# Optimization experiments

Measured on AMD Instinct MI355X. Metric: run time of the kernel, lower is better.

Reference implementation:

```python
import jax, jax.numpy as jnp
import numpy as np

B = 65536          # batch
H_DIM, W_DIM = 8, 8  # feather_size tuple
N = H_DIM * W_DIM    # 64 flat features
INNER = (N + 1) ** 2 # 4225 = outer-product size after prepending ones column
EPS = 1e-6


def setup_inputs() -> dict:
    key = jax.random.key(0)
    k1, k2 = jax.random.split(key, 2)
    x = jax.random.normal(k1, (B, N), jnp.float32)
    # nn.Linear(INNER, N): weight [out, in] = [N, INNER]
    W = jax.random.normal(k2, (N, INNER), jnp.float32) / np.sqrt(INNER)
    b = jnp.zeros((N,), jnp.float32)
    gamma = jnp.ones((N,), jnp.float32)   # LayerNorm scale
    beta = jnp.zeros((N,), jnp.float32)   # LayerNorm shift
    return {"x": x, "W": W, "b": b, "gamma": gamma, "beta": beta}


def reference(x, W, b, gamma, beta):
    Bsz = x.shape[0]
    # prepend ones column: [B, N+1]
    ones = jnp.ones((Bsz, 1), x.dtype)
    x1 = jnp.concatenate([ones, x], axis=-1)
    # bmm outer product x1 @ x1^T per row -> [B, N+1, N+1], flatten to [B, INNER]
    outer = (x1[:, :, None] * x1[:, None, :]).reshape(Bsz, INNER)
    # Linear(INNER -> N)
    y = outer @ W.T + b  # [B, N]
    # UER-py LayerNorm: gamma*(y-u)/sqrt(var+eps)+beta over last dim
    u = jnp.mean(y, axis=-1, keepdims=True)
    s = jnp.mean((y - u) ** 2, axis=-1, keepdims=True)
    y = gamma * (y - u) / jnp.sqrt(s + EPS) + beta
    # final view back to the (out) feather matrix shape
    return y.reshape(Bsz, H_DIM, W_DIM)
```

## Files before the change

### kernel.cpp

```cpp
#include <hip/hip_runtime.h>
#include <stdint.h>
#include <stddef.h>

typedef _Float16 f16;
typedef _Float16 f16x2 __attribute__((ext_vector_type(2)));
typedef _Float16 f16x4 __attribute__((ext_vector_type(4)));
typedef _Float16 f16x8 __attribute__((ext_vector_type(8)));
typedef float f32x16 __attribute__((ext_vector_type(16)));

#define INNER_SZ 4225
#define NQ 164
#define XSTR 72

__global__ __launch_bounds__(256) void cm_prep(const float* __restrict__ W,
                                               const float* __restrict__ bias,
                                               f16* __restrict__ Wf2,
                                               float* __restrict__ cvec) {
  int idx = blockIdx.x * 256 + threadIdx.x;
  if (idx < NQ * 1024) {
    int q   = idx >> 10;
    int r10 = idx & 1023;
    int ngh = r10 >> 9;
    int rr  = r10 & 511;
    int G   = rr >> 3;
    int e   = rr & 7;
    int c = G >> 1, hh = G & 1;
    int o = ngh * 32 + c;
    int kl = hh * 8 + e;
    float v = 0.f;
    if (q < 160) {
      int b, start;
      if (q < 16)      { b = 0; start = 0;  }
      else if (q < 48) { b = 1; start = 16; }
      else if (q < 96) { b = 2; start = 48; }
      else             { b = 3; start = 96; }
      int rel = q - start;
      int i = 16 * b + rel / (b + 1);
      int s = rel % (b + 1);
      int j = s * 16 + kl;
      if (j < i)
        v = W[o * INNER_SZ + (i + 1) * 65 + (j + 1)] +
            W[o * INNER_SZ + (j + 1) * 65 + (i + 1)];
      else if (j == i)
        v = W[o * INNER_SZ + (i + 1) * 65 + (i + 1)];
    } else {
      int j = (q - 160) * 16 + kl;
      v = W[o * INNER_SZ + (j + 1)] + W[o * INNER_SZ + (j + 1) * 65];
    }
    Wf2[idx] = (f16)v;
  }
  if (idx < 64) cvec[idx] = W[idx * INNER_SZ] + bias[idx];
}

__device__ __forceinline__ f16x8 mulsp(f16x2 sp, f16x8 wv) {
  f16x8 r;
#pragma unroll
  for (int e = 0; e < 4; ++e)
    ((f16x2*)&r)[e] = sp * ((const f16x2*)&wv)[e];
  return r;
}

template <int QLO>
__device__ __forceinline__ void kbody(f16x8 (&wr)[10], const char* bsrc,
                                      const f16* xs, int r0, int r1,
                                      const f16x8 (&xw0)[4], const f16x8 (&xw1)[4],
                                      f32x16& acc0, f32x16& acc1) {
  f16x2 sp0 = {}, sp1 = {};
#pragma unroll
  for (int qi = 0; qi < 82; ++qi) {
    const int q = QLO + qi;
    int i, s, lin;
    if (q >= 160) { i = 0; s = q - 160; lin = 1; }
    else {
      int b = (q < 16) ? 0 : (q < 48) ? 1 : (q < 96) ? 2 : 3;
      int st = (b == 0) ? 0 : (b == 1) ? 16 : (b == 2) ? 48 : 96;
      int rel = q - st;
      i = 16 * b + rel / (b + 1);
      s = rel % (b + 1);
      lin = 0;
    }
    bool newi = (qi == 0);
    if (qi > 0 && !lin) {
      int qp = q - 1;
      int bp = (qp < 16) ? 0 : (qp < 48) ? 1 : (qp < 96) ? 2 : 3;
      int stp = (bp == 0) ? 0 : (bp == 1) ? 16 : (bp == 2) ? 48 : 96;
      int ip = 16 * bp + (qp - stp) / (bp + 1);
      newi = (ip != i);
    }
    if (!lin && newi) {
      uint32_t u0 = *(const uint16_t*)(xs + r0 * XSTR + i);
      uint32_t u1 = *(const uint16_t*)(xs + r1 * XSTR + i);
      sp0 = __builtin_bit_cast(f16x2, u0 | (u0 << 16));
      sp1 = __builtin_bit_cast(f16x2, u1 | (u1 << 16));
    }
    f16x8 b_ = wr[qi % 10];
    if (qi + 10 < 82)
      wr[qi % 10] = *(const f16x8*)(bsrc + (size_t)(QLO + qi + 10) * 2048);
    f16x8 a0, a1;
    if (lin) { a0 = xw0[s]; a1 = xw1[s]; }
    else     { a0 = mulsp(sp0, xw0[s]); a1 = mulsp(sp1, xw1[s]); }
    acc0 = __builtin_amdgcn_mfma_f32_32x32x16_f16(a0, b_, acc0, 0, 0, 0);
    acc1 = __builtin_amdgcn_mfma_f32_32x32x16_f16(a1, b_, acc1, 0, 0, 0);
  }
}

__global__ __launch_bounds__(512, 4) void cm_main(
    const float* __restrict__ x, const f16* __restrict__ Wf2,
    const float* __restrict__ cvec, const float* __restrict__ gamma,
    const float* __restrict__ beta, float* __restrict__ out) {
  __shared__ __align__(16) union SM {
    f16 xs[128 * XSTR];
    struct { float red[128][64]; float yt[64 * 128]; } e;
  } sm;

  const int tid = threadIdx.x;
  const int lane = tid & 63;
  const int w = tid >> 6;
  const int rowg = w & 1;
  const int ch = (w >> 1) & 1;
  const int seg = w >> 2;
  const int c31 = lane & 31;
  const int h = lane >> 5;
  const long mbase = (long)blockIdx.x * 128;

  const char* bsrc = (const char*)Wf2 + ch * 1024 + (2 * c31 + h) * 16;
  f16x8 wr[10];
  if (seg == 0) {
#pragma unroll
    for (int p = 0; p < 10; ++p)
      wr[p] = *(const f16x8*)(bsrc + (size_t)p * 2048);
  } else {
#pragma unroll
    for (int p = 0; p < 10; ++p)
      wr[p] = *(const f16x8*)(bsrc + (size_t)(82 + p) * 2048);
  }

#pragma unroll
  for (int it = 0; it < 4; ++it) {
    int idx = it * 2048 + tid * 4;
    int row = idx >> 6, col = idx & 63;
    const float4 v = *(const float4*)(x + (size_t)(mbase + row) * 64 + col);
    f16x4 hv = {(f16)v.x, (f16)v.y, (f16)v.z, (f16)v.w};
    *(f16x4*)(sm.xs + row * XSTR + col) = hv;
  }
  __syncthreads();

  const int r0 = rowg * 64 + c31, r1 = rowg * 64 + 32 + c31;
  f16x8 xw0[4], xw1[4];
#pragma unroll
  for (int s = 0; s < 4; ++s) {
    xw0[s] = *(const f16x8*)(sm.xs + r0 * XSTR + s * 16 + h * 8);
    xw1[s] = *(const f16x8*)(sm.xs + r1 * XSTR + s * 16 + h * 8);
  }

  f32x16 acc0 = (f32x16)(0.0f);
  f32x16 acc1 = (f32x16)(0.0f);
  if (seg == 0) kbody<0>(wr, bsrc, sm.xs, r0, r1, xw0, xw1, acc0, acc1);
  else          kbody<82>(wr, bsrc, sm.xs, r0, r1, xw0, xw1, acc0, acc1);

  __syncthreads();
  if (seg == 1) {
#pragma unroll
    for (int r = 0; r < 16; ++r) {
      int rl = (r & 3) + 8 * (r >> 2) + 4 * h;
      sm.e.red[rowg * 64 + rl][ch * 32 + c31] = acc0[r];
      sm.e.red[rowg * 64 + 32 + rl][ch * 32 + c31] = acc1[r];
    }
  }
  __syncthreads();
  if (seg == 0) {
#pragma unroll
    for (int r = 0; r < 16; ++r) {
      int rl = (r & 3) + 8 * (r >> 2) + 4 * h;
      acc0[r] += sm.e.red[rowg * 64 + rl][ch * 32 + c31];
      acc1[r] += sm.e.red[rowg * 64 + 32 + rl][ch * 32 + c31];
    }
    const int cg = ch * 32 + c31;
    const int swz = (c31 & 7) << 4;
#pragma unroll
    for (int rq = 0; rq < 4; ++rq) {
      int b0 = cg * 512 + rowg * 256 + 0 * 128 + rq * 32 + h * 16;
      int b1 = cg * 512 + rowg * 256 + 1 * 128 + rq * 32 + h * 16;
      *(float4*)((char*)sm.e.yt + (b0 ^ swz)) =
          make_float4(acc0[rq * 4 + 0], acc0[rq * 4 + 1], acc0[rq * 4 + 2], acc0[rq * 4 + 3]);
      *(float4*)((char*)sm.e.yt + (b1 ^ swz)) =
          make_float4(acc1[rq * 4 + 0], acc1[rq * 4 + 1], acc1[rq * 4 + 2], acc1[rq * 4 + 3]);
    }
  }
  __syncthreads();

  if (tid < 256) {
    int row = tid >> 1, half = tid & 1;
    float y[32];
    float s = 0.f, qs = 0.f;
#pragma unroll
    for (int j = 0; j < 32; ++j) {
      int c = half * 32 + j;
      int byte = (c * 512 + row * 4) ^ ((c & 7) << 4);
      float v = *(const float*)((const char*)sm.e.yt + byte);
      v += cvec[c];
      y[j] = v;
      s += v; qs += v * v;
    }
    s  += __shfl_xor(s, 1);
    qs += __shfl_xor(qs, 1);
    float mean = s * 0.015625f;
    float var = qs * 0.015625f - mean * mean;
    float rstd = rsqrtf(var + 1e-6f);
#pragma unroll
    for (int j = 0; j < 32; ++j) {
      int c = half * 32 + j;
      y[j] = gamma[c] * (y[j] - mean) * rstd + beta[c];
    }
    float* op = out + (size_t)(mbase + row) * 64 + half * 32;
#pragma unroll
    for (int j4 = 0; j4 < 8; ++j4)
      *(float4*)(op + j4 * 4) =
          make_float4(y[j4 * 4 + 0], y[j4 * 4 + 1], y[j4 * 4 + 2], y[j4 * 4 + 3]);
  }
}

extern "C" void kernel_launch(void* const* d_in, const int* in_sizes, int n_in,
                              void* d_out, int out_size, void* d_ws, size_t ws_size,
                              hipStream_t stream) {
  const float* x     = (const float*)d_in[0];
  const float* W     = (const float*)d_in[1];
  const float* bias  = (const float*)d_in[2];
  const float* gamma = (const float*)d_in[3];
  const float* beta  = (const float*)d_in[4];
  float* out = (float*)d_out;

  f16* Wf2 = (f16*)d_ws;
  float* cvec = (float*)((char*)d_ws + NQ * 1024 * 2);

  cm_prep<<<(NQ * 1024 + 255) / 256, 256, 0, stream>>>(W, bias, Wf2, cvec);
  cm_main<<<512, 512, 0, stream>>>(x, Wf2, cvec, gamma, beta, out);
}
```

Baseline: 37.96 us.

## Use inline-asm triple-buffered weight loads and shuffle-based x scalar fetch

Replaces the 10-deep compiler-managed register prefetch of weight fragments with a 3-deep ring of inline-asm global loads and explicit vmcnt waits before each MFMA pair. Separately, the per-row scalar x value that was re-read from LDS is now pulled from the already-loaded xw registers, taking the value from the other half-wave via a lane-xor-32 shuffle. This is meant to cut VGPR pressure and LDS traffic inside the main loop. The risk is that a shallower prefetch exposes more global-load latency, and that the shuffles add extra cross-lane operations.

```diff
diff --git a/kernel.cpp b/kernel.cpp
--- a/kernel.cpp
+++ b/kernel.cpp
@@ -7,6 +7,8 @@
 typedef _Float16 f16x4 __attribute__((ext_vector_type(4)));
 typedef _Float16 f16x8 __attribute__((ext_vector_type(8)));
 typedef float f32x16 __attribute__((ext_vector_type(16)));
+typedef uint32_t u32x4 __attribute__((ext_vector_type(4)));
+typedef int i32x4 __attribute__((ext_vector_type(4)));
 
 #define INNER_SZ 4225
 #define NQ 164
@@ -61,10 +63,15 @@
 }
 
 template <int QLO>
-__device__ __forceinline__ void kbody(f16x8 (&wr)[10], const char* bsrc,
-                                      const f16* xs, int r0, int r1,
-                                      const f16x8 (&xw0)[4], const f16x8 (&xw1)[4],
+__device__ __forceinline__ void kbody(const char* bsrc, int h,
+                                      f16x8 (&xw0)[4], f16x8 (&xw1)[4],
                                       f32x16& acc0, f32x16& acc1) {
+  i32x4 vb[3];
+#pragma unroll
+  for (int p = 0; p < 3; ++p)
+    asm volatile("global_load_dwordx4 %0, %1, off"
+                 : "=v"(vb[p])
+                 : "v"(bsrc + (size_t)(QLO + p) * 2048));
   f16x2 sp0 = {}, sp1 = {};
 #pragma unroll
   for (int qi = 0; qi < 82; ++qi) {
@@ -88,19 +95,35 @@
       newi = (ip != i);
     }
     if (!lin && newi) {
-      uint32_t u0 = *(const uint16_t*)(xs + r0 * XSTR + i);
-      uint32_t u1 = *(const uint16_t*)(xs + r1 * XSTR + i);
-      sp0 = __builtin_bit_cast(f16x2, u0 | (u0 << 16));
-      sp1 = __builtin_bit_cast(f16x2, u1 | (u1 << 16));
-    }
-    f16x8 b_ = wr[qi % 10];
-    if (qi + 10 < 82)
-      wr[qi % 10] = *(const f16x8*)(bsrc + (size_t)(QLO + qi + 10) * 2048);
+      const int si = i >> 4, hb = (i >> 3) & 1, wd = (i & 7) >> 1, pp = i & 1;
+      uint32_t ow0 = __builtin_bit_cast(u32x4, xw0[si])[wd];
+      uint32_t ow1 = __builtin_bit_cast(u32x4, xw1[si])[wd];
+      uint32_t pw0 = (uint32_t)__shfl_xor((int)ow0, 32, 64);
+      uint32_t pw1 = (uint32_t)__shfl_xor((int)ow1, 32, 64);
+      uint32_t sel0 = (h == hb) ? ow0 : pw0;
+      uint32_t sel1 = (h == hb) ? ow1 : pw1;
+      uint32_t v0 = pp ? (sel0 >> 16) : (sel0 & 0xffffu);
+      uint32_t v1 = pp ? (sel1 >> 16) : (sel1 & 0xffffu);
+      sp0 = __builtin_bit_cast(f16x2, v0 | (v0 << 16));
+      sp1 = __builtin_bit_cast(f16x2, v1 | (v1 << 16));
+    }
     f16x8 a0, a1;
     if (lin) { a0 = xw0[s]; a1 = xw1[s]; }
     else     { a0 = mulsp(sp0, xw0[s]); a1 = mulsp(sp1, xw1[s]); }
+    {
+      const int out = (81 - qi < 2) ? (81 - qi) : 2;
+      if (out == 2)      asm volatile("s_waitcnt vmcnt(2)" ::: "memory");
+      else if (out == 1) asm volatile("s_waitcnt vmcnt(1)" ::: "memory");
+      else               asm volatile("s_waitcnt vmcnt(0)" ::: "memory");
+      __builtin_amdgcn_sched_barrier(0);
+    }
+    f16x8 b_ = __builtin_bit_cast(f16x8, vb[qi % 3]);
     acc0 = __builtin_amdgcn_mfma_f32_32x32x16_f16(a0, b_, acc0, 0, 0, 0);
     acc1 = __builtin_amdgcn_mfma_f32_32x32x16_f16(a1, b_, acc1, 0, 0, 0);
+    if (qi + 3 < 82)
+      asm volatile("global_load_dwordx4 %0, %1, off"
+                   : "=v"(vb[qi % 3])
+                   : "v"(bsrc + (size_t)(q + 3) * 2048));
   }
 }
 
@@ -124,16 +147,6 @@
   const long mbase = (long)blockIdx.x * 128;
 
   const char* bsrc = (const char*)Wf2 + ch * 1024 + (2 * c31 + h) * 16;
-  f16x8 wr[10];
-  if (seg == 0) {
-#pragma unroll
-    for (int p = 0; p < 10; ++p)
-      wr[p] = *(const f16x8*)(bsrc + (size_t)p * 2048);
-  } else {
-#pragma unroll
-    for (int p = 0; p < 10; ++p)
-      wr[p] = *(const f16x8*)(bsrc + (size_t)(82 + p) * 2048);
-  }
 
 #pragma unroll
   for (int it = 0; it < 4; ++it) {
@@ -152,11 +165,14 @@
     xw0[s] = *(const f16x8*)(sm.xs + r0 * XSTR + s * 16 + h * 8);
     xw1[s] = *(const f16x8*)(sm.xs + r1 * XSTR + s * 16 + h * 8);
   }
+#pragma unroll
+  for (int s = 0; s < 4; ++s)
+    asm volatile("" : "+v"(xw0[s]), "+v"(xw1[s]));
 
   f32x16 acc0 = (f32x16)(0.0f);
   f32x16 acc1 = (f32x16)(0.0f);
-  if (seg == 0) kbody<0>(wr, bsrc, sm.xs, r0, r1, xw0, xw1, acc0, acc1);
-  else          kbody<82>(wr, bsrc, sm.xs, r0, r1, xw0, xw1, acc0, acc1);
+  if (seg == 0) kbody<0>(bsrc, h, xw0, xw1, acc0, acc1);
+  else          kbody<82>(bsrc, h, xw0, xw1, acc0, acc1);
 
   __syncthreads();
   if (seg == 1) {
```

New measurement: 37.88 us. About the same (-0.2%).

## Stream weights through double-buffered LDS ring with async global-to-LDS loads

Applied to the files above, without the earlier changes.

Drops the K-split across two wave segments, which needed a cross-segment reduction through shared memory, and halves the block to 256 threads. The weight fragments are now staged with global_load_lds into a two-slot LDS ring, one phase ahead, with a barrier per phase. Each wave reads its B fragments from LDS instead of holding a 10-deep register prefetch, and the per-row x scalar is prefetched one step ahead. This cuts register pressure and global traffic, since weights are shared across waves through LDS, but adds 41 block barriers and leaves fewer waves per block to hide latency.

```diff
diff --git a/kernel.cpp b/kernel.cpp
--- a/kernel.cpp
+++ b/kernel.cpp
@@ -11,6 +11,7 @@
 #define INNER_SZ 4225
 #define NQ 164
 #define XSTR 72
+#define NPH 41
 
 __global__ __launch_bounds__(256) void cm_prep(const float* __restrict__ W,
                                                const float* __restrict__ bias,
@@ -52,6 +53,12 @@
   if (idx < 64) cvec[idx] = W[idx * INNER_SZ] + bias[idx];
 }
 
+__device__ inline void gload_lds16(const void* gp, void* lp) {
+  __builtin_amdgcn_global_load_lds(
+      (const __attribute__((address_space(1))) uint32_t*)(uintptr_t)gp,
+      (__attribute__((address_space(3))) uint32_t*)(uintptr_t)lp, 16, 0, 0);
+}
+
 __device__ __forceinline__ f16x8 mulsp(f16x2 sp, f16x8 wv) {
   f16x8 r;
 #pragma unroll
@@ -60,88 +67,44 @@
   return r;
 }
 
-template <int QLO>
-__device__ __forceinline__ void kbody(f16x8 (&wr)[10], const char* bsrc,
-                                      const f16* xs, int r0, int r1,
-                                      const f16x8 (&xw0)[4], const f16x8 (&xw1)[4],
-                                      f32x16& acc0, f32x16& acc1) {
-  f16x2 sp0 = {}, sp1 = {};
-#pragma unroll
-  for (int qi = 0; qi < 82; ++qi) {
-    const int q = QLO + qi;
-    int i, s, lin;
-    if (q >= 160) { i = 0; s = q - 160; lin = 1; }
-    else {
-      int b = (q < 16) ? 0 : (q < 48) ? 1 : (q < 96) ? 2 : 3;
-      int st = (b == 0) ? 0 : (b == 1) ? 16 : (b == 2) ? 48 : 96;
-      int rel = q - st;
-      i = 16 * b + rel / (b + 1);
-      s = rel % (b + 1);
-      lin = 0;
-    }
-    bool newi = (qi == 0);
-    if (qi > 0 && !lin) {
-      int qp = q - 1;
-      int bp = (qp < 16) ? 0 : (qp < 48) ? 1 : (qp < 96) ? 2 : 3;
-      int stp = (bp == 0) ? 0 : (bp == 1) ? 16 : (bp == 2) ? 48 : 96;
-      int ip = 16 * bp + (qp - stp) / (bp + 1);
-      newi = (ip != i);
-    }
-    if (!lin && newi) {
-      uint32_t u0 = *(const uint16_t*)(xs + r0 * XSTR + i);
-      uint32_t u1 = *(const uint16_t*)(xs + r1 * XSTR + i);
-      sp0 = __builtin_bit_cast(f16x2, u0 | (u0 << 16));
-      sp1 = __builtin_bit_cast(f16x2, u1 | (u1 << 16));
-    }
-    f16x8 b_ = wr[qi % 10];
-    if (qi + 10 < 82)
-      wr[qi % 10] = *(const f16x8*)(bsrc + (size_t)(QLO + qi + 10) * 2048);
-    f16x8 a0, a1;
-    if (lin) { a0 = xw0[s]; a1 = xw1[s]; }
-    else     { a0 = mulsp(sp0, xw0[s]); a1 = mulsp(sp1, xw1[s]); }
-    acc0 = __builtin_amdgcn_mfma_f32_32x32x16_f16(a0, b_, acc0, 0, 0, 0);
-    acc1 = __builtin_amdgcn_mfma_f32_32x32x16_f16(a1, b_, acc1, 0, 0, 0);
-  }
-}
-
-__global__ __launch_bounds__(512, 4) void cm_main(
+__global__ __launch_bounds__(256, 4) void cm_main(
     const float* __restrict__ x, const f16* __restrict__ Wf2,
     const float* __restrict__ cvec, const float* __restrict__ gamma,
     const float* __restrict__ beta, float* __restrict__ out) {
   __shared__ __align__(16) union SM {
-    f16 xs[128 * XSTR];
-    struct { float red[128][64]; float yt[64 * 128]; } e;
+    struct { f16 ring[2][4096]; f16 xs[128 * XSTR]; } k;
+    float yt[8192];
   } sm;
 
   const int tid = threadIdx.x;
   const int lane = tid & 63;
   const int w = tid >> 6;
   const int rowg = w & 1;
-  const int ch = (w >> 1) & 1;
-  const int seg = w >> 2;
+  const int ch = w >> 1;
   const int c31 = lane & 31;
   const int h = lane >> 5;
   const long mbase = (long)blockIdx.x * 128;
 
-  const char* bsrc = (const char*)Wf2 + ch * 1024 + (2 * c31 + h) * 16;
-  f16x8 wr[10];
-  if (seg == 0) {
-#pragma unroll
-    for (int p = 0; p < 10; ++p)
-      wr[p] = *(const f16x8*)(bsrc + (size_t)p * 2048);
-  } else {
-#pragma unroll
-    for (int p = 0; p < 10; ++p)
-      wr[p] = *(const f16x8*)(bsrc + (size_t)(82 + p) * 2048);
-  }
-
-#pragma unroll
-  for (int it = 0; it < 4; ++it) {
-    int idx = it * 2048 + tid * 4;
+  const char* wsrc = (const char*)Wf2 + lane * 16;
+  char* ringb = (char*)&sm.k.ring[0][0];
+
+#define STAGE2(P)                                                           \
+  do {                                                                      \
+    const char* s_ = wsrc + (size_t)(4 * (P) + w) * 2048;                   \
+    char* d_ = ringb + (((P) & 1) ? 8192 : 0) + w * 2048;                   \
+    gload_lds16(s_, d_);                                                    \
+    gload_lds16(s_ + 1024, d_ + 1024);                                      \
+  } while (0)
+
+  STAGE2(0);
+
+#pragma unroll
+  for (int it = 0; it < 8; ++it) {
+    int idx = it * 1024 + tid * 4;
     int row = idx >> 6, col = idx & 63;
     const float4 v = *(const float4*)(x + (size_t)(mbase + row) * 64 + col);
     f16x4 hv = {(f16)v.x, (f16)v.y, (f16)v.z, (f16)v.w};
-    *(f16x4*)(sm.xs + row * XSTR + col) = hv;
+    *(f16x4*)(sm.k.xs + row * XSTR + col) = hv;
   }
   __syncthreads();
 
@@ -149,47 +112,82 @@
   f16x8 xw0[4], xw1[4];
 #pragma unroll
   for (int s = 0; s < 4; ++s) {
-    xw0[s] = *(const f16x8*)(sm.xs + r0 * XSTR + s * 16 + h * 8);
-    xw1[s] = *(const f16x8*)(sm.xs + r1 * XSTR + s * 16 + h * 8);
-  }
+    xw0[s] = *(const f16x8*)(sm.k.xs + r0 * XSTR + s * 16 + h * 8);
+    xw1[s] = *(const f16x8*)(sm.k.xs + r1 * XSTR + s * 16 + h * 8);
+  }
+#pragma unroll
+  for (int s = 0; s < 4; ++s)
+    asm volatile("" : "+v"(xw0[s]), "+v"(xw1[s]));
+
+  const int bfo = ch * 1024 + (2 * c31 + h) * 16;
 
   f32x16 acc0 = (f32x16)(0.0f);
   f32x16 acc1 = (f32x16)(0.0f);
-  if (seg == 0) kbody<0>(wr, bsrc, sm.xs, r0, r1, xw0, xw1, acc0, acc1);
-  else          kbody<82>(wr, bsrc, sm.xs, r0, r1, xw0, xw1, acc0, acc1);
-
-  __syncthreads();
-  if (seg == 1) {
-#pragma unroll
-    for (int r = 0; r < 16; ++r) {
-      int rl = (r & 3) + 8 * (r >> 2) + 4 * h;
-      sm.e.red[rowg * 64 + rl][ch * 32 + c31] = acc0[r];
-      sm.e.red[rowg * 64 + 32 + rl][ch * 32 + c31] = acc1[r];
-    }
-  }
-  __syncthreads();
-  if (seg == 0) {
-#pragma unroll
-    for (int r = 0; r < 16; ++r) {
-      int rl = (r & 3) + 8 * (r >> 2) + 4 * h;
-      acc0[r] += sm.e.red[rowg * 64 + rl][ch * 32 + c31];
-      acc1[r] += sm.e.red[rowg * 64 + 32 + rl][ch * 32 + c31];
-    }
+  uint32_t un0 = *(const uint16_t*)(sm.k.xs + r0 * XSTR);
+  uint32_t un1 = *(const uint16_t*)(sm.k.xs + r1 * XSTR);
+  f16x2 sp0 = {}, sp1 = {};
+
+#pragma unroll
+  for (int p = 0; p < NPH; ++p) {
+    if (p + 1 < NPH) STAGE2(p + 1);
+    const char* rb = ringb + ((p & 1) ? 8192 : 0);
+#pragma unroll
+    for (int kk = 0; kk < 4; ++kk) {
+      const int q = 4 * p + kk;
+      int i, s, lin;
+      if (q >= 160) { i = 64; s = q - 160; lin = 1; }
+      else {
+        int b = (q < 16) ? 0 : (q < 48) ? 1 : (q < 96) ? 2 : 3;
+        int st = (b == 0) ? 0 : (b == 1) ? 16 : (b == 2) ? 48 : 96;
+        int rel = q - st;
+        i = 16 * b + rel / (b + 1);
+        s = rel % (b + 1);
+        lin = 0;
+      }
+      bool newi;
+      if (q == 0) newi = true;
+      else if (lin) newi = false;
+      else {
+        int qp = q - 1;
+        int bp = (qp < 16) ? 0 : (qp < 48) ? 1 : (qp < 96) ? 2 : 3;
+        int stp = (bp == 0) ? 0 : (bp == 1) ? 16 : (bp == 2) ? 48 : 96;
+        newi = (16 * bp + (qp - stp) / (bp + 1)) != i;
+      }
+      if (newi) {
+        uint32_t u0 = un0 & 0xffffu, u1 = un1 & 0xffffu;
+        sp0 = __builtin_bit_cast(f16x2, u0 | (u0 << 16));
+        sp1 = __builtin_bit_cast(f16x2, u1 | (u1 << 16));
+        if (i + 1 < 64) {
+          un0 = *(const uint16_t*)(sm.k.xs + r0 * XSTR + i + 1);
+          un1 = *(const uint16_t*)(sm.k.xs + r1 * XSTR + i + 1);
+        }
+      }
+      f16x8 bf = *(const f16x8*)(rb + kk * 2048 + bfo);
+      f16x8 a0, a1;
+      if (lin) { a0 = xw0[s]; a1 = xw1[s]; }
+      else     { a0 = mulsp(sp0, xw0[s]); a1 = mulsp(sp1, xw1[s]); }
+      acc0 = __builtin_amdgcn_mfma_f32_32x32x16_f16(a0, bf, acc0, 0, 0, 0);
+      acc1 = __builtin_amdgcn_mfma_f32_32x32x16_f16(a1, bf, acc1, 0, 0, 0);
+    }
+    __syncthreads();
+  }
+
+  {
     const int cg = ch * 32 + c31;
     const int swz = (c31 & 7) << 4;
 #pragma unroll
     for (int rq = 0; rq < 4; ++rq) {
       int b0 = cg * 512 + rowg * 256 + 0 * 128 + rq * 32 + h * 16;
       int b1 = cg * 512 + rowg * 256 + 1 * 128 + rq * 32 + h * 16;
-      *(float4*)((char*)sm.e.yt + (b0 ^ swz)) =
+      *(float4*)((char*)sm.yt + (b0 ^ swz)) =
           make_float4(acc0[rq * 4 + 0], acc0[rq * 4 + 1], acc0[rq * 4 + 2], acc0[rq * 4 + 3]);
-      *(float4*)((char*)sm.e.yt + (b1 ^ swz)) =
+      *(float4*)((char*)sm.yt + (b1 ^ swz)) =
           make_float4(acc1[rq * 4 + 0], acc1[rq * 4 + 1], acc1[rq * 4 + 2], acc1[rq * 4 + 3]);
     }
   }
   __syncthreads();
 
-  if (tid < 256) {
+  {
     int row = tid >> 1, half = tid & 1;
     float y[32];
     float s = 0.f, qs = 0.f;
@@ -197,7 +195,7 @@
     for (int j = 0; j < 32; ++j) {
       int c = half * 32 + j;
       int byte = (c * 512 + row * 4) ^ ((c & 7) << 4);
-      float v = *(const float*)((const char*)sm.e.yt + byte);
+      float v = *(const float*)((const char*)sm.yt + byte);
       v += cvec[c];
       y[j] = v;
       s += v; qs += v * v;
@@ -218,6 +216,7 @@
       *(float4*)(op + j4 * 4) =
           make_float4(y[j4 * 4 + 0], y[j4 * 4 + 1], y[j4 * 4 + 2], y[j4 * 4 + 3]);
   }
+#undef STAGE2
 }
 
 extern "C" void kernel_launch(void* const* d_in, const int* in_sizes, int n_in,
@@ -234,5 +233,5 @@
   float* cvec = (float*)((char*)d_ws + NQ * 1024 * 2);
 
   cm_prep<<<(NQ * 1024 + 255) / 256, 256, 0, stream>>>(W, bias, Wf2, cvec);
-  cm_main<<<512, 512, 0, stream>>>(x, Wf2, cvec, gamma, beta, out);
-}
+  cm_main<<<512, 256, 0, stream>>>(x, Wf2, cvec, gamma, beta, out);
+}
```

After: 39.57 us. 1.04x slower.
